# Kernel optimization log

Hardware: AMD Instinct MI355X
Metric: run time of the kernel (lower is better)

The kernel has to match this reference:

```python
import jax, jax.numpy as jnp
import numpy as np

K = 8192            # codebook_size
DECAY = 0.99        # ema_decay
COMMIT = 0.25       # commitment_cost
ENT_RATIO = 0.1     # entropy_loss_ratio
ENT_TEMP = 1.0      # entropy_temperature
EPS = 1e-5


def setup_inputs() -> dict:
    key = jax.random.key(0)
    k1, k2, k3, k4 = jax.random.split(key, 4)
    x = jax.random.normal(k1, (32768, 256), dtype=jnp.float32)
    codebook = jax.random.normal(k2, (8192, 256), dtype=jnp.float32)
    cluster_size_ema = jax.random.uniform(k3, (8192,), dtype=jnp.float32)
    codebook_ema = jax.random.normal(k4, (8192, 256), dtype=jnp.float32)
    return {"x": x, "codebook": codebook,
            "cluster_size_ema": cluster_size_ema, "codebook_ema": codebook_ema}


def _entropy_loss(affinity, temperature):
    # affinity: [N, K]
    a = affinity / temperature
    probs = jax.nn.softmax(a, axis=-1)
    log_probs = jax.nn.log_softmax(a + 1e-5, axis=-1)
    avg_probs = jnp.mean(probs, axis=0)                      # [K]
    avg_entropy = -jnp.sum(avg_probs * jnp.log(avg_probs + 1e-5))
    sample_entropy = -jnp.mean(jnp.sum(probs * log_probs, axis=-1))
    return sample_entropy - avg_entropy


def reference(x, codebook, cluster_size_ema, codebook_ema):
    N, d = x.shape
    x2 = jnp.sum(x * x, axis=1, keepdims=True)               # [N,1]
    c2 = jnp.sum(codebook * codebook, axis=1)                # [K]
    d2 = x2 - 2.0 * (x @ codebook.T) + c2[None, :]           # [N,K]
    distances = jnp.sqrt(jnp.maximum(d2, 0.0))
    encoding_indices = jnp.argmin(distances, axis=1)         # [N]
    quantized = codebook[encoding_indices]                   # [N,d]

    # training losses (straight-through for output)
    e_latent_loss = jnp.mean((jax.lax.stop_gradient(quantized) - x) ** 2) * COMMIT
    q_latent_loss = jnp.mean((quantized - jax.lax.stop_gradient(x)) ** 2)
    ent = _entropy_loss(-distances, ENT_TEMP) * ENT_RATIO
    loss = e_latent_loss + q_latent_loss + ent

    # EMA codebook update (encodings.sum(0) and encodings^T @ x via segment sums)
    counts = jax.ops.segment_sum(jnp.ones((N,), x.dtype), encoding_indices,
                                 num_segments=K)             # [K]
    dw = jax.ops.segment_sum(x, encoding_indices, num_segments=K)  # [K,d]
    new_cluster_size_ema = DECAY * cluster_size_ema + (1.0 - DECAY) * counts
    new_codebook_ema = DECAY * codebook_ema + (1.0 - DECAY) * dw
    n = jnp.sum(new_cluster_size_ema)
    smoothed = (new_cluster_size_ema + EPS) / (n + K * EPS) * n
    new_codebook = new_codebook_ema / smoothed[:, None]

    quantized_st = x + jax.lax.stop_gradient(quantized - x)

    avg_probs = counts / N
    perplexity = jnp.exp(-jnp.sum(avg_probs * jnp.log(avg_probs + 1e-10)))

    return (quantized_st, loss, perplexity, encoding_indices,
            new_codebook, new_cluster_size_ema, new_codebook_ema)
```

## Files before the change

kernel.cpp:

```cpp
#include <hip/hip_runtime.h>
#include <math.h>

#define N_ROWS 32768
#define DIM 256
#define KCODES 8192

#define BM 128
#define BN 128
#define NSLICE 8
#define SLICE_K 1024
#define NKT (SLICE_K / BN)
#define NDT 4
#define NSTEP (NKT * NDT)
#define TAU 3e-3f

#define FAST_SQRT(x) __builtin_amdgcn_sqrtf(x)

#define WS_C2    0
#define WS_X2    8192
#define WS_BD    40960
#define WS_BI    73728
#define WS_L     106496
#define WS_FLAGL 139264
#define WS_AVGP  172032
#define WS_CNT   180224
#define WS_SCAL  188416
#define WS_FLAGN 188424

#define PF (NSLICE * N_ROWS)

typedef _Float16 f16x8 __attribute__((ext_vector_type(8)));
typedef float f32x4 __attribute__((ext_vector_type(4)));

__device__ __forceinline__ void gll16(const void* g, void* l) {
    __builtin_amdgcn_global_load_lds((const __attribute__((address_space(1))) void*)g,
                                     (__attribute__((address_space(3))) void*)l, 16, 0, 0);
}

__global__ void split_k(const float* __restrict__ src, ushort* __restrict__ h,
                        float* __restrict__ norms) {
    int tid = threadIdx.x;
    int i = blockIdx.x * 256 + tid;
    const float4* s4 = (const float4*)src;
    float4 v0 = s4[2 * i], v1 = s4[2 * i + 1];
    float vv[8] = {v0.x, v0.y, v0.z, v0.w, v1.x, v1.y, v1.z, v1.w};
    float nrm = 0.f;
    uint w[4];
    #pragma unroll
    for (int p = 0; p < 4; ++p) {
        float a = vv[2*p], b = vv[2*p+1];
        nrm = fmaf(a, a, nrm); nrm = fmaf(b, b, nrm);
        _Float16 ha = (_Float16)a, hb = (_Float16)b;
        w[p] = (uint)__builtin_bit_cast(unsigned short, ha)
             | ((uint)__builtin_bit_cast(unsigned short, hb) << 16);
    }
    ((uint4*)h)[i] = make_uint4(w[0], w[1], w[2], w[3]);
    #pragma unroll
    for (int off = 16; off >= 1; off >>= 1) nrm += __shfl_xor(nrm, off);
    if ((tid & 31) == 0) norms[blockIdx.x * 8 + (tid >> 5)] = nrm;
}

__global__ void init_ncbe_k(const float* __restrict__ cbe, float* __restrict__ outNcbe) {
    int i = blockIdx.x * 256 + threadIdx.x;
    float4 v = ((const float4*)cbe)[i];
    v.x *= 0.99f; v.y *= 0.99f; v.z *= 0.99f; v.w *= 0.99f;
    ((float4*)outNcbe)[i] = v;
}

__device__ __forceinline__ void online_merge(float& b1, int& i1, float& b2, float& l, float& T,
                                             float nb1, int ni1, float nb2, float nl, float nT) {
    float m  = fminf(b1, nb1);
    float fa = __expf(m - b1);
    float fb = __expf(m - nb1);
    float L  = fa * l + fb * nl;
    float TT = fa * (T + (m - b1) * l) + fb * (nT + (m - nb1) * nl);
    float losing = fmaxf(b1, nb1);
    float B2 = fminf(fminf(b2, nb2), losing);
    if (nb1 < b1 || (nb1 == b1 && ni1 < i1)) i1 = ni1;
    b1 = m; b2 = B2; l = L; T = TT;
}

template<int PASS>
__global__ __launch_bounds__(512, 4) void vq_mfma(const ushort* __restrict__ xf,
                                                  const ushort* __restrict__ cf,
                                                  float* __restrict__ ws,
                                                  float* __restrict__ P) {
    __shared__ __align__(16) char lds[2][32768];
    __shared__ __align__(16) float c2s[SLICE_K];
    __shared__ float sred[1536];

    const int tid  = threadIdx.x;
    const int lane = tid & 63, wid = tid >> 6;
    const int wcode = wid & 1, wx = wid >> 1;
    const int l15 = lane & 15, l4 = lane >> 4;
    const int slice = blockIdx.x & 7, chunk = blockIdx.x >> 3;
    const int rowBase = chunk * BM;

    c2s[tid]       = ws[WS_C2 + slice * SLICE_K + tid];
    c2s[tid + 512] = ws[WS_C2 + slice * SLICE_K + tid + 512];
    if (PASS == 2) { sred[tid] = 0.f; sred[tid + 512] = 0.f; }

    const char* cbB[2]; const char* xB[2]; int dCB[2], dX[2];
    #pragma unroll
    for (int j = 0; j < 2; ++j) {
        int q = j * 512 + tid;
        int row = q >> 3, c = tid & 7;
        int sw = (c ^ (row & 7)) << 4;
        cbB[j] = (const char*)cf + (((size_t)(slice * SLICE_K + row)) << 9) + sw;
        xB[j]  = (const char*)xf + (((size_t)(rowBase + row)) << 9) + sw;
        dCB[j] = q << 4;
        dX[j]  = 16384 + (q << 4);
    }

    float x2v[2], bdv[2], invl[2];
    #pragma unroll
    for (int n = 0; n < 2; ++n) {
        int rl = wx * 32 + n * 16 + l15;
        x2v[n] = ws[WS_X2 + rowBase + rl];
        if (PASS == 2) {
            bdv[n]  = ws[WS_BD + rowBase + rl];
            invl[n] = 1.0f / ws[WS_L + rowBase + rl];
        }
    }
    float rb1[2], rb2[2], rlv[2], rTv[2]; int ri1[2];
    #pragma unroll
    for (int n = 0; n < 2; ++n) { rb1[n] = 1e30f; rb2[n] = 1e30f; rlv[n] = 0.f; rTv[n] = 0.f; ri1[n] = 0; }

    #pragma unroll
    for (int j = 0; j < 2; ++j) {
        gll16(cbB[j], &lds[0][dCB[j]]);
        gll16(xB[j],  &lds[0][dX[j]]);
    }

    const int swkey = l15 & 7;

    for (int kt = 0; kt < NKT; ++kt) {
        f32x4 acc[4][2];
        #pragma unroll
        for (int m = 0; m < 4; ++m) {
            acc[m][0] = (f32x4){0.f, 0.f, 0.f, 0.f};
            acc[m][1] = (f32x4){0.f, 0.f, 0.f, 0.f};
        }

        #pragma unroll
        for (int dt = 0; dt < NDT; ++dt) {
            const int t = kt * 4 + dt;
            if (t + 1 < NSTEP) {
                const int t1 = t + 1;
                const int cbo = ((t1 >> 2) << 16) | ((t1 & 3) << 7);
                const int xo  = (t1 & 3) << 7;
                char* wb = &lds[t1 & 1][0];
                #pragma unroll
                for (int j = 0; j < 2; ++j) {
                    gll16(cbB[j] + cbo, wb + dCB[j]);
                    gll16(xB[j] + xo,   wb + dX[j]);
                }
                asm volatile("s_waitcnt vmcnt(4)" ::: "memory");
            } else {
                asm volatile("s_waitcnt vmcnt(0)" ::: "memory");
            }
            __builtin_amdgcn_s_barrier();
            __builtin_amdgcn_sched_barrier(0);

            const char* bb = &lds[t & 1][0];
            #pragma unroll
            for (int s = 0; s < 2; ++s) {
                const int csw = (((s << 2) | l4) ^ swkey) << 4;
                f16x8 Bf[2];
                #pragma unroll
                for (int n = 0; n < 2; ++n)
                    Bf[n] = __builtin_bit_cast(f16x8,
                        *(const uint4*)(bb + 16384 + (wx * 32 + n * 16 + l15) * 128 + csw));
                __builtin_amdgcn_s_setprio(1);
                #pragma unroll
                for (int m = 0; m < 4; ++m) {
                    f16x8 Af = __builtin_bit_cast(f16x8,
                        *(const uint4*)(bb + (wcode * 64 + m * 16 + l15) * 128 + csw));
                    acc[m][0] = __builtin_amdgcn_mfma_f32_16x16x32_f16(Af, Bf[0], acc[m][0], 0, 0, 0);
                    acc[m][1] = __builtin_amdgcn_mfma_f32_16x16x32_f16(Af, Bf[1], acc[m][1], 0, 0, 0);
                }
                __builtin_amdgcn_s_setprio(0);
            }
            __builtin_amdgcn_sched_barrier(0);
            __builtin_amdgcn_s_barrier();
        }

        const int cb0 = slice * SLICE_K + kt * BN + wcode * 64 + l4 * 4;
        const int lc0 = kt * BN + wcode * 64 + l4 * 4;
        if (PASS == 1) {
            #pragma unroll
            for (int n = 0; n < 2; ++n) {
                #pragma unroll
                for (int m = 0; m < 4; ++m) {
                    float4 c2v = *(const float4*)&c2s[lc0 + m * 16];
                    float dsv[4];
                    float b1 = 1e30f, b2 = 1e30f; int i1 = 0;
                    #pragma unroll
                    for (int r = 0; r < 4; ++r) {
                        float d2 = fmaf(-2.f, acc[m][n][r], x2v[n] + ((const float*)&c2v)[r]);
                        float dv = FAST_SQRT(fmaxf(d2, 0.f));
                        dsv[r] = dv;
                        bool better = dv < b1;
                        b2 = better ? b1 : fminf(b2, dv);
                        if (better) { b1 = dv; i1 = cb0 + m * 16 + r; }
                    }
                    float ls = 0.f, ts = 0.f;
                    #pragma unroll
                    for (int r = 0; r < 4; ++r) {
                        float e = __expf(b1 - dsv[r]);
                        ls += e;
                        ts = fmaf(e, b1 - dsv[r], ts);
                    }
                    online_merge(rb1[n], ri1[n], rb2[n], rlv[n], rTv[n], b1, i1, b2, ls, ts);
                }
            }
        } else {
            float ps[4][4];
            #pragma unroll
            for (int m = 0; m < 4; ++m)
                #pragma unroll
                for (int r = 0; r < 4; ++r) ps[m][r] = 0.f;
            #pragma unroll
            for (int n = 0; n < 2; ++n) {
                #pragma unroll
                for (int m = 0; m < 4; ++m) {
                    float4 c2v = *(const float4*)&c2s[lc0 + m * 16];
                    #pragma unroll
                    for (int r = 0; r < 4; ++r) {
                        float d2 = fmaf(-2.f, acc[m][n][r], x2v[n] + ((const float*)&c2v)[r]);
                        float dv = FAST_SQRT(fmaxf(d2, 0.f));
                        ps[m][r] = fmaf(__expf(bdv[n] - dv), invl[n], ps[m][r]);
                    }
                }
            }
            #pragma unroll
            for (int m = 0; m < 4; ++m)
                #pragma unroll
                for (int r = 0; r < 4; ++r) {
                    float v = ps[m][r];
                    v += __shfl_xor(v, 1); v += __shfl_xor(v, 2);
                    v += __shfl_xor(v, 4); v += __shfl_xor(v, 8);
                    ps[m][r] = v;
                }
            if (l15 == 0) {
                #pragma unroll
                for (int m = 0; m < 4; ++m)
                    #pragma unroll
                    for (int r = 0; r < 4; ++r)
                        atomicAdd(&sred[lc0 + m * 16 + r], ps[m][r]);
            }
        }
    }

    if (PASS == 1) {
        #pragma unroll
        for (int n = 0; n < 2; ++n) {
            #pragma unroll
            for (int off = 16; off <= 32; off <<= 1) {
                float ob1 = __shfl_xor(rb1[n], off);
                int   oi  = __shfl_xor(ri1[n], off);
                float ob2 = __shfl_xor(rb2[n], off);
                float ol  = __shfl_xor(rlv[n], off);
                float oT  = __shfl_xor(rTv[n], off);
                online_merge(rb1[n], ri1[n], rb2[n], rlv[n], rTv[n], ob1, oi, ob2, ol, oT);
            }
        }
        if (l4 == 0) {
            #pragma unroll
            for (int n = 0; n < 2; ++n) {
                int rl = wx * 32 + n * 16 + l15;
                sred[(rl << 1) + wcode]       = rb1[n];
                sred[256 + (rl << 1) + wcode] = rb2[n];
                sred[512 + (rl << 1) + wcode] = rlv[n];
                sred[768 + (rl << 1) + wcode] = rTv[n];
                ((int*)sred)[1024 + (rl << 1) + wcode] = ri1[n];
            }
        }
        __syncthreads();
        if (tid < BM) {
            float b1 = sred[tid * 2];       int i1 = ((int*)sred)[1024 + tid * 2];
            float b2 = sred[256 + tid * 2];
            float L  = sred[512 + tid * 2];
            float T  = sred[768 + tid * 2];
            online_merge(b1, i1, b2, L, T,
                         sred[tid * 2 + 1], ((int*)sred)[1024 + tid * 2 + 1],
                         sred[256 + tid * 2 + 1], sred[512 + tid * 2 + 1], sred[768 + tid * 2 + 1]);
            int grow = rowBase + tid;
            P[0 * PF + slice * N_ROWS + grow] = b1;
            P[1 * PF + slice * N_ROWS + grow] = b2;
            P[2 * PF + slice * N_ROWS + grow] = L;
            P[3 * PF + slice * N_ROWS + grow] = T;
            ((int*)P)[4 * PF + slice * N_ROWS + grow] = i1;
        }
    } else {
        __syncthreads();
        atomicAdd(&ws[WS_AVGP + slice * SLICE_K + tid], sred[tid]);
        atomicAdd(&ws[WS_AVGP + slice * SLICE_K + tid + 512], sred[tid + 512]);
    }
}

__global__ void merge_k(const float* __restrict__ P, float* __restrict__ ws,
                        unsigned long long* __restrict__ enc) {
    const int tid = threadIdx.x, lane = tid & 63;
    const int row = blockIdx.x * 256 + tid;
    float b1 = 1e30f, b2 = 1e30f, L = 0.f, T = 0.f; int i1 = 0;
    #pragma unroll
    for (int s = 0; s < NSLICE; ++s) {
        float nb1 = P[0 * PF + s * N_ROWS + row];
        float nb2 = P[1 * PF + s * N_ROWS + row];
        float nl  = P[2 * PF + s * N_ROWS + row];
        float nT  = P[3 * PF + s * N_ROWS + row];
        int   ni  = ((const int*)P)[4 * PF + s * N_ROWS + row];
        online_merge(b1, i1, b2, L, T, nb1, ni, nb2, nl, nT);
    }
    ws[WS_BD + row] = b1;
    ((int*)ws)[WS_BI + row] = i1;
    ws[WS_L + row] = L;
    if (b2 - b1 < TAU) {
        int p = atomicAdd(((int*)ws) + WS_FLAGN, 1);
        ((int*)ws)[WS_FLAGL + p] = row;
        enc[p] = ~0ULL;
    }
    float sval = T / L - __logf(L);
    #pragma unroll
    for (int off = 32; off >= 1; off >>= 1) sval += __shfl_xor(sval, off);
    if (lane == 0) atomicAdd(&ws[WS_SCAL + 1], sval);
}

__global__ __launch_bounds__(256) void fixup_k(const float* __restrict__ x,
                                               const float* __restrict__ cb,
                                               float* __restrict__ ws,
                                               unsigned long long* __restrict__ enc) {
    __shared__ __align__(16) float xrow[DIM];
    const int tid = threadIdx.x, lane = tid & 63, wid = tid >> 6;
    const int slice = blockIdx.x & 7;
    const int nf = ((const int*)ws)[WS_FLAGN];
    const int c0 = slice * SLICE_K + wid * 256;
    for (int fi = blockIdx.x >> 3; fi < nf; fi += (gridDim.x >> 3)) {
        const int row = ((const int*)ws)[WS_FLAGL + fi];
        __syncthreads();
        if (tid < 64) ((float4*)xrow)[tid] = ((const float4*)(x + (size_t)row * DIM))[tid];
        __syncthreads();
        const float x2r = ws[WS_X2 + row];
        const float4 xv = ((const float4*)xrow)[lane];
        unsigned long long best = ~0ULL;
        for (int j = 0; j < 256; ++j) {
            const int c = c0 + j;
            float4 cv = ((const float4*)(cb + (size_t)c * DIM))[lane];
            float dot = cv.x * xv.x;
            dot = fmaf(cv.y, xv.y, dot);
            dot = fmaf(cv.z, xv.z, dot);
            dot = fmaf(cv.w, xv.w, dot);
            #pragma unroll
            for (int off = 1; off <= 32; off <<= 1) dot += __shfl_xor(dot, off);
            float d2 = fmaxf(fmaf(-2.f, dot, x2r + ws[WS_C2 + c]), 0.f);
            float dv = sqrtf(d2);
            unsigned long long e = (((unsigned long long)__float_as_uint(dv)) << 32)
                                 | (unsigned int)c;
            best = (e < best) ? e : best;
        }
        if (lane == 0) atomicMin(&enc[fi], best);
    }
}

__global__ void unpack_k(const unsigned long long* __restrict__ enc, float* __restrict__ ws) {
    int f = blockIdx.x * 256 + threadIdx.x;
    int nf = ((const int*)ws)[WS_FLAGN];
    if (f < nf) {
        int row = ((const int*)ws)[WS_FLAGL + f];
        ((int*)ws)[WS_BI + row] = (int)(enc[f] & 0xFFFFFFFFu);
    }
}

__global__ void gather_k(const float* __restrict__ x, const float* __restrict__ cb,
                         float* __restrict__ ws, float* __restrict__ outQ,
                         float* __restrict__ outNcbe, float* __restrict__ outIdxF) {
    __shared__ float red2[4];
    const int tid = threadIdx.x, w = tid >> 6, lane = tid & 63;
    float msum = 0.f;
    for (int it = 0; it < 8; ++it) {
        int n = blockIdx.x * 32 + it * 4 + w;
        int idx = ((const int*)ws)[WS_BI + n];
        float4 xv = ((const float4*)(x + (size_t)n * DIM))[lane];
        float4 cv = ((const float4*)(cb + (size_t)idx * DIM))[lane];
        ((float4*)(outQ + (size_t)n * DIM))[lane] = cv;
        float* dst = outNcbe + (size_t)idx * DIM + lane * 4;
        const float g = 0.01f;
        atomicAdd(dst + 0, g * xv.x); atomicAdd(dst + 1, g * xv.y);
        atomicAdd(dst + 2, g * xv.z); atomicAdd(dst + 3, g * xv.w);
        float dx = cv.x - xv.x, dy = cv.y - xv.y, dz = cv.z - xv.z, dw = cv.w - xv.w;
        float s = dx*dx + dy*dy + dz*dz + dw*dw;
        #pragma unroll
        for (int off = 32; off >= 1; off >>= 1) s += __shfl_xor(s, off);
        if (lane == 0) {
            msum += s;
            atomicAdd(&ws[WS_CNT + idx], 1.0f);
            outIdxF[n] = (float)idx;
        }
    }
    if (lane == 0) red2[w] = msum;
    __syncthreads();
    if (tid == 0) atomicAdd(&ws[WS_SCAL + 0], red2[0] + red2[1] + red2[2] + red2[3]);
}

__global__ void stats_k(const float* __restrict__ cse, float* __restrict__ ws,
                        float* __restrict__ outNcse) {
    int tid = threadIdx.x, lane = tid & 63;
    int k = blockIdx.x * 256 + tid;
    float cnt = ws[WS_CNT + k];
    float ncse = 0.99f * cse[k] + 0.01f * cnt;
    outNcse[k] = ncse;
    float ap  = ws[WS_AVGP + k] * (1.0f / N_ROWS);
    float ae  = -(ap * __logf(ap + 1e-5f));
    float app = cnt * (1.0f / N_ROWS);
    float pe  = -(app * __logf(app + 1e-10f));
    #pragma unroll
    for (int off = 32; off >= 1; off >>= 1) {
        ncse += __shfl_xor(ncse, off);
        ae   += __shfl_xor(ae, off);
        pe   += __shfl_xor(pe, off);
    }
    if (lane == 0) {
        atomicAdd(&ws[WS_SCAL + 4], ncse);
        atomicAdd(&ws[WS_SCAL + 2], ae);
        atomicAdd(&ws[WS_SCAL + 3], pe);
    }
}

__global__ void newcb_k(const float* __restrict__ ws, const float* __restrict__ outNcse,
                        const float* __restrict__ outNcbe, float* __restrict__ outNc) {
    int w = threadIdx.x >> 6, lane = threadIdx.x & 63;
    int k = blockIdx.x * 4 + w;
    float n = ws[WS_SCAL + 4];
    float ncse = outNcse[k];
    float smoothed = (ncse + 1e-5f) / (n + (float)KCODES * 1e-5f) * n;
    float inv = 1.0f / smoothed;
    float4 v = ((const float4*)(outNcbe + (size_t)k * DIM))[lane];
    v.x *= inv; v.y *= inv; v.z *= inv; v.w *= inv;
    ((float4*)(outNc + (size_t)k * DIM))[lane] = v;
}

__global__ void finalize_k(const float* __restrict__ ws, float* __restrict__ outLoss,
                           float* __restrict__ outPerp) {
    float mse  = ws[WS_SCAL + 0] * (1.0f / ((float)N_ROWS * 256.0f));
    float sent = -ws[WS_SCAL + 1] * (1.0f / (float)N_ROWS);
    float ent  = sent - ws[WS_SCAL + 2];
    outLoss[0] = 1.25f * mse + 0.1f * ent;
    outPerp[0] = expf(ws[WS_SCAL + 3]);
}

extern "C" void kernel_launch(void* const* d_in, const int* in_sizes, int n_in,
                              void* d_out, int out_size, void* d_ws, size_t ws_size,
                              hipStream_t stream) {
    const float* x   = (const float*)d_in[0];
    const float* cb  = (const float*)d_in[1];
    const float* cse = (const float*)d_in[2];
    const float* cbe = (const float*)d_in[3];
    float* out = (float*)d_out;
    float* ws  = (float*)d_ws;

    float* outQ    = out;
    float* outLoss = out + 8388608;
    float* outPerp = out + 8388609;
    float* outIdxF = out + 8388610;
    float* outNc   = out + 8421378;
    float* outNcse = out + 10518530;
    float* outNcbe = out + 10526722;

    ushort* xf = (ushort*)outQ;
    ushort* cf = (ushort*)(out + 8421380);
    float*  P  = outNcbe;
    unsigned long long* enc = (unsigned long long*)(outNcbe + 5 * PF);

    (void)hipMemsetAsync(ws + WS_AVGP, 0, (size_t)(WS_FLAGN + 1 - WS_AVGP) * sizeof(float), stream);
    split_k<<<N_ROWS * DIM / 2048, 256, 0, stream>>>(x, xf, ws + WS_X2);
    split_k<<<KCODES * DIM / 2048, 256, 0, stream>>>(cb, cf, ws + WS_C2);
    vq_mfma<1><<<NSLICE * (N_ROWS / BM), 512, 0, stream>>>(xf, cf, ws, P);
    merge_k<<<N_ROWS / 256, 256, 0, stream>>>(P, ws, enc);
    vq_mfma<2><<<NSLICE * (N_ROWS / BM), 512, 0, stream>>>(xf, cf, ws, P);
    fixup_k<<<2048, 256, 0, stream>>>(x, cb, ws, enc);
    unpack_k<<<N_ROWS / 256, 256, 0, stream>>>(enc, ws);
    init_ncbe_k<<<2048, 256, 0, stream>>>(cbe, outNcbe);
    gather_k<<<1024, 256, 0, stream>>>(x, cb, ws, outQ, outNcbe, outIdxF);
    stats_k<<<KCODES / 256, 256, 0, stream>>>(cse, ws, outNcse);
    newcb_k<<<KCODES / 4, 256, 0, stream>>>(ws, outNcse, outNcbe, outNc);
    finalize_k<<<1, 1, 0, stream>>>(ws, outLoss, outPerp);
}
```

Before: 1.067 ms.

## Halve LDS stage size, raise occupancy, and pack distance-index argmin

Staging now uses 32-wide d-chunks with 8 steps per code tile, which halves the LDS double buffer and uses a new 4-column XOR swizzle. Launch bounds rise to 6 blocks per CU to gain occupancy. The pass-1 argmin packs the distance and local index into one uint, so a single top-2 scan covers 16 values per row with one online merge per tile instead of four. The cost is twice as many barrier-separated pipeline steps and truncated distance mantissas in the packed compare, which TAU is widened to absorb.

After: 1.786 ms. +67.4%, slower.

```diff
diff --git a/kernel.cpp b/kernel.cpp
--- a/kernel.cpp
+++ b/kernel.cpp
@@ -10,9 +10,9 @@
 #define NSLICE 8
 #define SLICE_K 1024
 #define NKT (SLICE_K / BN)
-#define NDT 4
+#define NDT 8
 #define NSTEP (NKT * NDT)
-#define TAU 3e-3f
+#define TAU 7e-3f
 
 #define FAST_SQRT(x) __builtin_amdgcn_sqrtf(x)
 
@@ -81,11 +81,11 @@
 }
 
 template<int PASS>
-__global__ __launch_bounds__(512, 4) void vq_mfma(const ushort* __restrict__ xf,
+__global__ __launch_bounds__(512, 6) void vq_mfma(const ushort* __restrict__ xf,
                                                   const ushort* __restrict__ cf,
                                                   float* __restrict__ ws,
                                                   float* __restrict__ P) {
-    __shared__ __align__(16) char lds[2][32768];
+    __shared__ __align__(16) char lds[2][16384];
     __shared__ __align__(16) float c2s[SLICE_K];
     __shared__ float sred[1536];
 
@@ -100,16 +100,14 @@
     c2s[tid + 512] = ws[WS_C2 + slice * SLICE_K + tid + 512];
     if (PASS == 2) { sred[tid] = 0.f; sred[tid + 512] = 0.f; }
 
-    const char* cbB[2]; const char* xB[2]; int dCB[2], dX[2];
-    #pragma unroll
-    for (int j = 0; j < 2; ++j) {
-        int q = j * 512 + tid;
-        int row = q >> 3, c = tid & 7;
-        int sw = (c ^ (row & 7)) << 4;
-        cbB[j] = (const char*)cf + (((size_t)(slice * SLICE_K + row)) << 9) + sw;
-        xB[j]  = (const char*)xf + (((size_t)(rowBase + row)) << 9) + sw;
-        dCB[j] = q << 4;
-        dX[j]  = 16384 + (q << 4);
+    const char* cbB; const char* xB; int dCB, dX;
+    {
+        int row = tid >> 2, c = tid & 3;
+        int col = c ^ ((row >> 1) & 3);
+        cbB = (const char*)cf + (((size_t)(slice * SLICE_K + row)) << 9) + (col << 4);
+        xB  = (const char*)xf + (((size_t)(rowBase + row)) << 9) + (col << 4);
+        dCB = tid << 4;
+        dX  = 8192 + (tid << 4);
     }
 
     float x2v[2], bdv[2], invl[2];
@@ -126,13 +124,12 @@
     #pragma unroll
     for (int n = 0; n < 2; ++n) { rb1[n] = 1e30f; rb2[n] = 1e30f; rlv[n] = 0.f; rTv[n] = 0.f; ri1[n] = 0; }
 
-    #pragma unroll
-    for (int j = 0; j < 2; ++j) {
-        gll16(cbB[j], &lds[0][dCB[j]]);
-        gll16(xB[j],  &lds[0][dX[j]]);
-    }
-
-    const int swkey = l15 & 7;
+    gll16(cbB, &lds[0][dCB]);
+    gll16(xB,  &lds[0][dX]);
+
+    const int p = l4 ^ ((l15 >> 1) & 3);
+    const int a0 = (wcode * 64 + l15) * 64 + p * 16;
+    const int b0 = 8192 + (wx * 32 + l15) * 64 + p * 16;
 
     for (int kt = 0; kt < NKT; ++kt) {
         f32x4 acc[4][2];
@@ -144,18 +141,15 @@
 
         #pragma unroll
         for (int dt = 0; dt < NDT; ++dt) {
-            const int t = kt * 4 + dt;
+            const int t = kt * 8 + dt;
             if (t + 1 < NSTEP) {
                 const int t1 = t + 1;
-                const int cbo = ((t1 >> 2) << 16) | ((t1 & 3) << 7);
-                const int xo  = (t1 & 3) << 7;
+                const int cbo = ((t1 >> 3) << 16) | ((t1 & 7) << 6);
+                const int xo  = (t1 & 7) << 6;
                 char* wb = &lds[t1 & 1][0];
-                #pragma unroll
-                for (int j = 0; j < 2; ++j) {
-                    gll16(cbB[j] + cbo, wb + dCB[j]);
-                    gll16(xB[j] + xo,   wb + dX[j]);
-                }
-                asm volatile("s_waitcnt vmcnt(4)" ::: "memory");
+                gll16(cbB + cbo, wb + dCB);
+                gll16(xB + xo,   wb + dX);
+                asm volatile("s_waitcnt vmcnt(2)" ::: "memory");
             } else {
                 asm volatile("s_waitcnt vmcnt(0)" ::: "memory");
             }
@@ -163,91 +157,85 @@
             __builtin_amdgcn_sched_barrier(0);
 
             const char* bb = &lds[t & 1][0];
-            #pragma unroll
-            for (int s = 0; s < 2; ++s) {
-                const int csw = (((s << 2) | l4) ^ swkey) << 4;
-                f16x8 Bf[2];
-                #pragma unroll
-                for (int n = 0; n < 2; ++n)
-                    Bf[n] = __builtin_bit_cast(f16x8,
-                        *(const uint4*)(bb + 16384 + (wx * 32 + n * 16 + l15) * 128 + csw));
-                __builtin_amdgcn_s_setprio(1);
+            f16x8 Bf[2];
+            #pragma unroll
+            for (int n = 0; n < 2; ++n)
+                Bf[n] = __builtin_bit_cast(f16x8, *(const uint4*)(bb + b0 + n * 1024));
+            __builtin_amdgcn_s_setprio(1);
+            #pragma unroll
+            for (int m = 0; m < 4; ++m) {
+                f16x8 Af = __builtin_bit_cast(f16x8, *(const uint4*)(bb + a0 + m * 1024));
+                acc[m][0] = __builtin_amdgcn_mfma_f32_16x16x32_f16(Af, Bf[0], acc[m][0], 0, 0, 0);
+                acc[m][1] = __builtin_amdgcn_mfma_f32_16x16x32_f16(Af, Bf[1], acc[m][1], 0, 0, 0);
+            }
+            __builtin_amdgcn_s_setprio(0);
+            __builtin_amdgcn_sched_barrier(0);
+            __builtin_amdgcn_s_barrier();
+        }
+
+        const int lcb = kt * BN + wcode * 64 + l4 * 4;
+        if (PASS == 1) {
+            #pragma unroll
+            for (int n = 0; n < 2; ++n) {
+                uint pm = ~0u, p2 = ~0u;
+                float dsv[16];
                 #pragma unroll
                 for (int m = 0; m < 4; ++m) {
-                    f16x8 Af = __builtin_bit_cast(f16x8,
-                        *(const uint4*)(bb + (wcode * 64 + m * 16 + l15) * 128 + csw));
-                    acc[m][0] = __builtin_amdgcn_mfma_f32_16x16x32_f16(Af, Bf[0], acc[m][0], 0, 0, 0);
-                    acc[m][1] = __builtin_amdgcn_mfma_f32_16x16x32_f16(Af, Bf[1], acc[m][1], 0, 0, 0);
-                }
-                __builtin_amdgcn_s_setprio(0);
-            }
-            __builtin_amdgcn_sched_barrier(0);
-            __builtin_amdgcn_s_barrier();
-        }
-
-        const int cb0 = slice * SLICE_K + kt * BN + wcode * 64 + l4 * 4;
-        const int lc0 = kt * BN + wcode * 64 + l4 * 4;
-        if (PASS == 1) {
-            #pragma unroll
-            for (int n = 0; n < 2; ++n) {
-                #pragma unroll
-                for (int m = 0; m < 4; ++m) {
-                    float4 c2v = *(const float4*)&c2s[lc0 + m * 16];
-                    float dsv[4];
-                    float b1 = 1e30f, b2 = 1e30f; int i1 = 0;
+                    float4 c2v = *(const float4*)&c2s[lcb + m * 16];
                     #pragma unroll
                     for (int r = 0; r < 4; ++r) {
                         float d2 = fmaf(-2.f, acc[m][n][r], x2v[n] + ((const float*)&c2v)[r]);
                         float dv = FAST_SQRT(fmaxf(d2, 0.f));
-                        dsv[r] = dv;
-                        bool better = dv < b1;
-                        b2 = better ? b1 : fminf(b2, dv);
-                        if (better) { b1 = dv; i1 = cb0 + m * 16 + r; }
+                        dsv[m * 4 + r] = dv;
+                        uint pk = (__float_as_uint(dv) & 0xFFFFFC00u)
+                                | (uint)(lcb + m * 16 + r);
+                        bool lt = pk < pm;
+                        uint alt = (pk < p2) ? pk : p2;
+                        p2 = lt ? pm : alt;
+                        pm = lt ? pk : pm;
                     }
-                    float ls = 0.f, ts = 0.f;
-                    #pragma unroll
-                    for (int r = 0; r < 4; ++r) {
-                        float e = __expf(b1 - dsv[r]);
-                        ls += e;
-                        ts = fmaf(e, b1 - dsv[r], ts);
-                    }
-                    online_merge(rb1[n], ri1[n], rb2[n], rlv[n], rTv[n], b1, i1, b2, ls, ts);
                 }
+                float b1  = __uint_as_float(pm & 0xFFFFFC00u);
+                float b2v = __uint_as_float(p2 & 0xFFFFFC00u);
+                int   i1  = slice * SLICE_K + (int)(pm & 1023u);
+                float ls = 0.f, ts = 0.f;
+                #pragma unroll
+                for (int q = 0; q < 16; ++q) {
+                    float u = b1 - dsv[q];
+                    float e = __expf(u);
+                    ls += e;
+                    ts = fmaf(e, u, ts);
+                }
+                online_merge(rb1[n], ri1[n], rb2[n], rlv[n], rTv[n], b1, i1, b2v, ls, ts);
             }
         } else {
-            float ps[4][4];
-            #pragma unroll
-            for (int m = 0; m < 4; ++m)
-                #pragma unroll
-                for (int r = 0; r < 4; ++r) ps[m][r] = 0.f;
+            float ps[16];
+            #pragma unroll
+            for (int q = 0; q < 16; ++q) ps[q] = 0.f;
             #pragma unroll
             for (int n = 0; n < 2; ++n) {
                 #pragma unroll
                 for (int m = 0; m < 4; ++m) {
-                    float4 c2v = *(const float4*)&c2s[lc0 + m * 16];
+                    float4 c2v = *(const float4*)&c2s[lcb + m * 16];
                     #pragma unroll
                     for (int r = 0; r < 4; ++r) {
                         float d2 = fmaf(-2.f, acc[m][n][r], x2v[n] + ((const float*)&c2v)[r]);
                         float dv = FAST_SQRT(fmaxf(d2, 0.f));
-                        ps[m][r] = fmaf(__expf(bdv[n] - dv), invl[n], ps[m][r]);
+                        ps[m * 4 + r] = fmaf(__expf(bdv[n] - dv), invl[n], ps[m * 4 + r]);
                     }
                 }
             }
             #pragma unroll
-            for (int m = 0; m < 4; ++m)
-                #pragma unroll
-                for (int r = 0; r < 4; ++r) {
-                    float v = ps[m][r];
-                    v += __shfl_xor(v, 1); v += __shfl_xor(v, 2);
-                    v += __shfl_xor(v, 4); v += __shfl_xor(v, 8);
-                    ps[m][r] = v;
-                }
+            for (int q = 0; q < 16; ++q) {
+                float v = ps[q];
+                v += __shfl_xor(v, 1); v += __shfl_xor(v, 2);
+                v += __shfl_xor(v, 4); v += __shfl_xor(v, 8);
+                ps[q] = v;
+            }
             if (l15 == 0) {
                 #pragma unroll
-                for (int m = 0; m < 4; ++m)
-                    #pragma unroll
-                    for (int r = 0; r < 4; ++r)
-                        atomicAdd(&sred[lc0 + m * 16 + r], ps[m][r]);
+                for (int q = 0; q < 16; ++q)
+                    atomicAdd(&sred[lcb + (q >> 2) * 16 + (q & 3)], ps[q]);
             }
         }
     }
```
